# Optimization experiments

Measured on AMD Instinct MI355X. Metric: run time of the kernel, lower is better.

Reference implementation:

```python
import jax, jax.numpy as jnp
import numpy as np

# Model hyperparameters (from init_kwargs)
B, N, D = 64, 196, 768      # batch, patches, patch_dim
TKN = 768                   # token dim
QK = 64                     # per-head qk dim
H = 12                      # heads
HN = int(4.0 * TKN)         # Hopfield hidden = 3072
BETA = 1.0 / np.sqrt(QK)    # attn_beta default: 1/sqrt(qk_dim)
BLOCKS = 2
K_STEPS = 4                 # time_steps per block
EPS = 1e-5
ALPHA_RAW0 = float(np.log(np.exp(1.0) - 1.0))  # softplus^-1(alpha_init=1.0)


def setup_inputs() -> dict:
    key = jax.random.key(0)
    ks = jax.random.split(key, 8)
    sd = 0.02
    return {
        "x": jax.random.normal(ks[0], (B, N, D), dtype=jnp.float32),
        "W_enc": jax.random.normal(ks[1], (D, TKN), dtype=jnp.float32) * sd,
        "b_enc": jnp.zeros((TKN,), jnp.float32),
        "cls": jnp.ones((1, 1, TKN), jnp.float32),
        "pos": jax.random.normal(ks[2], (1, N + 1, TKN), dtype=jnp.float32) * sd,
        "gamma": jnp.ones((BLOCKS,), jnp.float32),             # EnergyLayerNorm scalar gain per block
        "bias": jnp.zeros((BLOCKS, TKN), jnp.float32),          # EnergyLayerNorm bias per block
        "Wq": jax.random.normal(ks[3], (BLOCKS, H, QK, TKN), dtype=jnp.float32) * sd,
        "Wk": jax.random.normal(ks[4], (BLOCKS, H, QK, TKN), dtype=jnp.float32) * sd,
        "Whn": jax.random.normal(ks[5], (BLOCKS, TKN, HN), dtype=jnp.float32) * sd,
        "alpha_raw": jnp.full((BLOCKS,), ALPHA_RAW0, jnp.float32),
        "ln_g": jnp.ones((TKN,), jnp.float32),
        "ln_b": jnp.zeros((TKN,), jnp.float32),
        "W_dec": jax.random.normal(ks[6], (TKN, D), dtype=jnp.float32) * sd,
        "b_dec": jnp.zeros((D,), jnp.float32),
    }


def _enorm(x, g_scale, g_bias):
    # EnergyLayerNorm: scalar gamma, per-dim bias, RMS of centered x
    xm = x - x.mean(-1, keepdims=True)
    return g_scale * xm * jax.lax.rsqrt((xm * xm).mean(-1, keepdims=True) + EPS) + g_bias


def _energy(g, Wq, Wk, Whn):
    # Hopfield-attention energy: -1/beta * sum logsumexp(beta * K^T Q)
    q = jnp.einsum("bnd,hzd->bnhz", g, Wq)
    k = jnp.einsum("bnd,hzd->bnhz", g, Wk)
    logits = jnp.einsum("bqhz,bkhz->bhqk", q, k)  # [B,H,N+1,N+1]
    e_attn = -(1.0 / BETA) * jnp.sum(jax.nn.logsumexp(BETA * logits, axis=-1))
    # Hopfield memory energy: -0.5 * sum relu(g W)^2
    e_hn = -0.5 * jnp.sum(jax.nn.relu(g @ Whn) ** 2)
    return e_attn + e_hn


_egrad = jax.grad(_energy)


def reference(x, W_enc, b_enc, cls, pos, gamma, bias, Wq, Wk, Whn, alpha_raw,
              ln_g, ln_b, W_dec, b_dec):
    t = x @ W_enc + b_enc                                   # encode -> [B,N,TKN]
    t = jnp.concatenate([jnp.broadcast_to(cls, (t.shape[0], 1, TKN)), t], axis=1)
    t = t + pos                                             # [B,N+1,TKN]
    for b in range(BLOCKS):
        a = jax.nn.softplus(alpha_raw[b])
        for _ in range(K_STEPS):
            g = _enorm(t, gamma[b], bias[b])
            t = t - a * _egrad(g, Wq[b], Wk[b], Whn[b])
    # decode: standard LayerNorm then Linear
    mu = t.mean(-1, keepdims=True)
    var = ((t - mu) ** 2).mean(-1, keepdims=True)
    h = (t - mu) * jax.lax.rsqrt(var + EPS) * ln_g + ln_b
    out = h @ W_dec + b_dec
    return out[:, 1:]                                       # drop CLS -> [B,N,D]
```

## Files before the change

### kernel.cpp

```cpp
#include <hip/hip_runtime.h>
#include <cstdint>
#include <cstddef>

using u16 = unsigned short;
typedef short short8 __attribute__((ext_vector_type(8)));
typedef short short4v __attribute__((ext_vector_type(4)));
typedef float f32x4 __attribute__((ext_vector_type(4)));

#define LN_EPS 1e-5f
#define ATT_BETA 0.125f

__device__ __forceinline__ u16 f2bf(float f){
  uint32_t u = __float_as_uint(f);
  u += 0x7fffu + ((u >> 16) & 1u);
  return (u16)(u >> 16);
}
__device__ __forceinline__ float bf2f(u16 h){
  return __uint_as_float(((uint32_t)h) << 16);
}
__device__ __forceinline__ float wred_sum(float v){
  #pragma unroll
  for(int o=32;o;o>>=1) v += __shfl_xor(v,o,64);
  return v;
}
__device__ __forceinline__ void async16(const void* g, void* l){
  __builtin_amdgcn_global_load_lds((const __attribute__((address_space(1))) void*)g,
                                   (__attribute__((address_space(3))) void*)l, 16, 0, 0);
}

template<int EPI, int ASPL>
__global__ __launch_bounds__(256)
void gemm_bt(const u16* __restrict__ A, const u16* __restrict__ A2,
             const u16* __restrict__ B,
             u16* __restrict__ Cb, float* __restrict__ Cf,
             int M, int N, int K, int ldb, int ldc,
             const float* __restrict__ aux0, const float* __restrict__ aux1,
             const float* __restrict__ araw, int blk)
{
  __shared__ u16 lA[128*32];
  __shared__ u16 lB[128*32];
  int tid = threadIdx.x;
  int w = tid >> 6, l = tid & 63;
  int wm = w >> 1, wn = w & 1;
  int m0 = blockIdx.y * 128, n0 = blockIdx.x * 128;
  int lr = l >> 2;
  int lc = (l & 3) * 8;
  f32x4 acc[4][4];
  #pragma unroll
  for(int i=0;i<4;i++)
    #pragma unroll
    for(int j=0;j<4;j++) acc[i][j] = (f32x4){0.f,0.f,0.f,0.f};
  int fm = l & 15, fq = (l >> 4) * 8;

  for(int kt=0; kt<K; kt+=32){
    __syncthreads();
    const u16* Asrc = A; int kcol = kt;
    if(ASPL){ if(kt >= 768){ Asrc = A2; kcol = kt - 768; } }
    int lda = ASPL ? 768 : K;
    #pragma unroll
    for(int c=0;c<2;c++){
      int rr = (w*2+c)*16;
      int ga = m0 + rr + lr; if(ga > M-1) ga = M-1;
      async16(Asrc + (size_t)ga*lda + kcol + lc, &lA[rr*32]);
      int gb = n0 + rr + lr; if(gb > N-1) gb = N-1;
      async16(B + (size_t)gb*ldb + kt + lc, &lB[rr*32]);
    }
    __syncthreads();
    short8 af[4], bfv[4];
    #pragma unroll
    for(int i=0;i<4;i++) af[i]  = *(const short8*)&lA[(wm*64 + i*16 + fm)*32 + fq];
    #pragma unroll
    for(int j=0;j<4;j++) bfv[j] = *(const short8*)&lB[(wn*64 + j*16 + fm)*32 + fq];
    #pragma unroll
    for(int i=0;i<4;i++)
      #pragma unroll
      for(int j=0;j<4;j++)
        acc[i][j] = __builtin_amdgcn_mfma_f32_16x16x32_bf16(af[i], bfv[j], acc[i][j], 0, 0, 0);
  }

  float alpha = 0.f;
  if(EPI==2) alpha = log1pf(__expf(araw[blk]));

  #pragma unroll
  for(int i=0;i<4;i++){
    int row_b = m0 + wm*64 + i*16 + (l>>4)*4;
    #pragma unroll
    for(int j=0;j<4;j++){
      int col = n0 + wn*64 + j*16 + (l&15);
      #pragma unroll
      for(int r=0;r<4;r++){
        int row = row_b + r;
        if(row >= M) continue;
        float v = acc[i][j][r];
        if(EPI==1){
          Cb[(size_t)row*ldc + col] = f2bf(v > 0.f ? v : 0.f);
        } else if(EPI==2){
          Cf[(size_t)row*768 + col] += alpha * v;
        } else if(EPI==3){
          int pb = row / 196, pn = row - pb*196;
          Cf[((size_t)pb*197 + 1 + pn)*768 + col] = v + aux0[col] + aux1[(size_t)(1+pn)*768 + col];
        } else {
          int pb = row / 197, rr2 = row - pb*197;
          if(rr2 > 0) Cf[((size_t)pb*196 + rr2 - 1)*768 + col] = v + aux0[col];
        }
      }
    }
  }
}

__global__ __launch_bounds__(256)
void norm_k(const float* __restrict__ t, u16* __restrict__ out,
            const float* __restrict__ gv, const float* __restrict__ bv, int blk, int mode)
{
  __shared__ float r1[4], r2[4];
  int row = blockIdx.x;
  const float* tr = t + (size_t)row*768;
  int tid = threadIdx.x, w = tid>>6, l = tid&63;
  f32x4 v = (f32x4){0.f,0.f,0.f,0.f};
  float s=0.f, s2=0.f;
  if(tid < 192){
    v = ((const f32x4*)tr)[tid];
    s  = v[0]+v[1]+v[2]+v[3];
    s2 = v[0]*v[0]+v[1]*v[1]+v[2]*v[2]+v[3]*v[3];
  }
  s = wred_sum(s); s2 = wred_sum(s2);
  if(l==0){ r1[w]=s; r2[w]=s2; }
  __syncthreads();
  s  = r1[0]+r1[1]+r1[2]+r1[3];
  s2 = r2[0]+r2[1]+r2[2]+r2[3];
  float mu  = s * (1.0f/768.0f);
  float var = s2 * (1.0f/768.0f) - mu*mu;
  float rs  = rsqrtf(var + LN_EPS);
  u16* orow = out + (size_t)row*768;
  if(tid < 192){
    short4v o;
    if(mode==0){
      float gm = gv[blk];
      const float* bb = bv + blk*768;
      #pragma unroll
      for(int c=0;c<4;c++) o[c] = (short)f2bf((v[c]-mu)*rs*gm + bb[tid*4+c]);
    } else {
      #pragma unroll
      for(int c=0;c<4;c++) o[c] = (short)f2bf((v[c]-mu)*rs*gv[tid*4+c] + bv[tid*4+c]);
    }
    ((short4v*)orow)[tid] = o;
  }
}

__global__ __launch_bounds__(512, 2)
void attn_fused(const u16* __restrict__ g, const u16* __restrict__ Wqk,
                u16* __restrict__ GqO, u16* __restrict__ GkO)
{
  __shared__ u16 smem[76800];
  __shared__ float SredS[2][4][16];
  u16* Qlds = smem;
  u16* Klds = smem + 14976;
  u16* QTl  = smem + 29952;
  u16* KTl  = smem + 44800;
  u16* P    = smem + 59648;
  u16* PT   = smem + 67840;
  u16* lg   = smem + 59648;

  int bhw = blockIdx.x;
  int bh = (bhw & 7)*96 + (bhw >> 3);
  int b = bh/12, h = bh - b*12;
  const u16* grows = g + (size_t)b*197*768;
  u16* Qg = GqO + (size_t)b*197*768 + h*64;
  u16* Kg = GkO + (size_t)b*197*768 + h*64;
  int tid = threadIdx.x, w = tid>>6, l = tid&63;
  int lane16 = l & 15, quad = l >> 4;

  for(int idx=tid; idx<64*24; idx+=512){
    int z = idx/24, c = 208 + (idx - (idx/24)*24);
    QTl[z*232 + c] = 0; KTl[z*232 + c] = 0;
  }

  {
    int half = w >> 2;
    int wsub = w & 3;
    int rt0 = (wsub==0) ? 0 : 1 + 3*wsub;
    int rtn = (wsub==0) ? 4 : 3;
    const u16* Wb = Wqk + (size_t)half*589824 + (size_t)(h*64)*768;
    u16* Lr = half ? Klds : Qlds;
    u16* Lt = half ? KTl  : QTl;
    f32x4 acc[4][4];
    #pragma unroll
    for(int i=0;i<4;i++)
      #pragma unroll
      for(int z=0;z<4;z++) acc[i][z] = (f32x4){0.f,0.f,0.f,0.f};

    #define STAGE_G(bufi, ktv) do{                                                   \
      int idx0 = tid;                                                                \
      { int rw = idx0>>2, c4 = idx0&3; int r2 = rw>196?196:rw;                       \
        async16(grows + (size_t)r2*768 + (ktv)*32 + c4*8, lg + (bufi)*6656 + idx0*8);}\
      int idx1 = tid + 512;                                                          \
      if(idx1 < 832){ int rw = idx1>>2, c4 = idx1&3; int r2 = rw>196?196:rw;         \
        async16(grows + (size_t)r2*768 + (ktv)*32 + c4*8, lg + (bufi)*6656 + idx1*8);}\
    }while(0)

    short8 bq[4], bqn[4];
    #pragma unroll
    for(int z=0;z<4;z++) bq[z] = *(const short8*)(Wb + (size_t)(z*16+lane16)*768 + quad*8);
    STAGE_G(0, 0);
    int buf = 0;
    for(int kt=0; kt<24; kt++){
      __syncthreads();
      if(kt < 23){
        STAGE_G(buf^1, kt+1);
        #pragma unroll
        for(int z=0;z<4;z++)
          bqn[z] = *(const short8*)(Wb + (size_t)(z*16+lane16)*768 + (kt+1)*32 + quad*8);
      }
      const u16* lb = lg + buf*6656;
      #pragma unroll
      for(int i=0;i<4;i++) if(i<rtn){
        short8 af = *(const short8*)(lb + (size_t)((rt0+i)*16 + lane16)*32 + quad*8);
        #pragma unroll
        for(int z=0;z<4;z++)
          acc[i][z] = __builtin_amdgcn_mfma_f32_16x16x32_bf16(af, bq[z], acc[i][z],0,0,0);
      }
      #pragma unroll
      for(int z=0;z<4;z++) bq[z] = bqn[z];
      buf ^= 1;
    }
    #undef STAGE_G

    #pragma unroll
    for(int i=0;i<4;i++) if(i<rtn)
      #pragma unroll
      for(int z=0;z<4;z++)
        #pragma unroll
        for(int r=0;r<4;r++){
          int q  = (rt0+i)*16 + quad*4 + r;
          int zz = z*16 + lane16;
          u16 hv = f2bf(acc[i][z][r]);
          Lr[q*72   + zz] = hv;
          Lt[zz*232 + q ] = hv;
        }
  }
  __syncthreads();

  int mt = w & 1, nh = w >> 1;
  int ncnt = (nh==0) ? 4 : 3;
  int nt0s = (nh==0) ? 0 : (1 + 3*nh);
  int jt0 = (w<5) ? 2*w : 10+(w-5);
  int jn  = (w<5) ? 2 : 1;

  f32x4 gk[2][4];
  #pragma unroll
  for(int a=0;a<2;a++)
    #pragma unroll
    for(int n2=0;n2<4;n2++) gk[a][n2] = (f32x4){0.f,0.f,0.f,0.f};

  for(int st=0; st<7; st++){
    int q0 = st*32;
    __syncthreads();
    int qa = q0 + 16*mt + lane16; if(qa > 196) qa = 196;
    short8 a0 = *(const short8*)&Qlds[qa*72 + quad*8];
    short8 a1 = *(const short8*)&Qlds[qa*72 + 32 + quad*8];
    f32x4 sa[4];
    #pragma unroll
    for(int ni=0;ni<4;ni++) sa[ni] = (f32x4){0.f,0.f,0.f,0.f};
    for(int ni=0; ni<ncnt; ni++){
      int jb = (nt0s+ni)*16 + lane16; if(jb > 196) jb = 196;
      short8 b0 = *(const short8*)&Klds[jb*72 + quad*8];
      short8 b1 = *(const short8*)&Klds[jb*72 + 32 + quad*8];
      sa[ni] = __builtin_amdgcn_mfma_f32_16x16x32_bf16(a0, b0, sa[ni],0,0,0);
      sa[ni] = __builtin_amdgcn_mfma_f32_16x16x32_bf16(a1, b1, sa[ni],0,0,0);
    }
    for(int ni=0; ni<ncnt; ni++){
      if((nt0s+ni)*16 + lane16 > 196){
        sa[ni][0]=-3e38f; sa[ni][1]=-3e38f; sa[ni][2]=-3e38f; sa[ni][3]=-3e38f;
      }
    }
    float ss[4] = {0.f,0.f,0.f,0.f};
    for(int ni=0; ni<ncnt; ni++)
      #pragma unroll
      for(int r=0;r<4;r++){
        float e = __expf(fminf(ATT_BETA*sa[ni][r], 80.f));
        sa[ni][r] = e; ss[r] += e;
      }
    #pragma unroll
    for(int o=1;o<16;o<<=1)
      #pragma unroll
      for(int r=0;r<4;r++) ss[r] += __shfl_xor(ss[r], o, 64);
    if(lane16==0){
      #pragma unroll
      for(int r=0;r<4;r++) SredS[mt][nh][quad*4+r] = ss[r];
    }
    __syncthreads();
    float inv[4];
    #pragma unroll
    for(int r=0;r<4;r++)
      inv[r] = 1.f/(SredS[mt][0][quad*4+r] + SredS[mt][1][quad*4+r]
                  + SredS[mt][2][quad*4+r] + SredS[mt][3][quad*4+r]);
    for(int ni=0; ni<ncnt; ni++){
      int j = (nt0s+ni)*16 + lane16;
      short4v pk;
      #pragma unroll
      for(int r=0;r<4;r++){
        int q = 16*mt + quad*4 + r;
        float val = (q0 + q <= 196) ? sa[ni][r]*inv[r] : 0.f;
        u16 hv = f2bf(val);
        P[q*256 + 8*((j>>3)^(q&7)) + (j&7)] = hv;
        pk[r] = (short)hv;
      }
      *(short4v*)&PT[j*40 + 16*mt + 4*quad] = pk;
    }
    for(int idx=tid; idx<32*16; idx+=512){
      int q = idx>>4, j = 208 + (idx&15);
      P[q*256 + 8*((j>>3)^(q&7)) + (j&7)] = 0;
    }
    __syncthreads();
    {
      f32x4 gq = (f32x4){0.f,0.f,0.f,0.f};
      int qrow = 16*mt + lane16;
      int z = nh*16 + lane16;
      for(int kt=0; kt<7; kt++){
        short8 af = *(const short8*)&P[qrow*256 + 8*((4*kt+quad)^(qrow&7))];
        short8 bf8 = *(const short8*)&KTl[z*232 + kt*32 + quad*8];
        gq = __builtin_amdgcn_mfma_f32_16x16x32_bf16(af, bf8, gq,0,0,0);
      }
      #pragma unroll
      for(int r=0;r<4;r++){
        int qg2 = q0 + 16*mt + quad*4 + r;
        if(qg2 <= 196) Qg[(size_t)qg2*768 + nh*16 + lane16] = f2bf(gq[r]);
      }
    }
    {
      short8 bq2[4];
      #pragma unroll
      for(int n2=0;n2<4;n2++)
        bq2[n2] = *(const short8*)&QTl[(n2*16+lane16)*232 + q0 + quad*8];
      for(int ji=0; ji<jn; ji++){
        int j = (jt0+ji)*16 + lane16;
        short8 af = *(const short8*)&PT[j*40 + quad*8];
        #pragma unroll
        for(int n2=0;n2<4;n2++)
          gk[ji][n2] = __builtin_amdgcn_mfma_f32_16x16x32_bf16(af, bq2[n2], gk[ji][n2],0,0,0);
      }
    }
  }
  __syncthreads();
  for(int ji=0; ji<jn; ji++){
    int jt = jt0 + ji;
    #pragma unroll
    for(int n2=0;n2<4;n2++)
      #pragma unroll
      for(int r=0;r<4;r++){
        int j = jt*16 + quad*4 + r;
        if(j <= 196) Kg[(size_t)j*768 + n2*16 + lane16] = f2bf(gk[ji][n2][r]);
      }
  }
}

__global__ void cvt_k(const float* __restrict__ in, u16* __restrict__ out, int n){
  for(int i=blockIdx.x*256+threadIdx.x; i<n; i+=gridDim.x*256) out[i] = f2bf(in[i]);
}

__global__ __launch_bounds__(256)
void tr_k(const float* __restrict__ src, u16* __restrict__ dst, int R, int C, int dstride, int coff){
  __shared__ float tile[32][33];
  int c0 = blockIdx.x*32, r0 = blockIdx.y*32;
  int tx = threadIdx.x & 31, ty = threadIdx.x >> 5;
  for(int i=ty;i<32;i+=8) tile[i][tx] = src[(size_t)(r0+i)*C + c0 + tx];
  __syncthreads();
  for(int i=ty;i<32;i+=8) dst[(size_t)(c0+i)*dstride + coff + r0 + tx] = f2bf(tile[tx][i]);
}

__global__ void fill_cls_k(float* __restrict__ t, const float* __restrict__ cls, const float* __restrict__ pos){
  int b = blockIdx.x;
  for(int i=threadIdx.x;i<768;i+=256) t[(size_t)b*197*768 + i] = cls[i] + pos[i];
}

extern "C" void kernel_launch(void* const* d_in, const int* in_sizes, int n_in,
                              void* d_out, int out_size, void* d_ws, size_t ws_size,
                              hipStream_t stream){
  const float* x      = (const float*)d_in[0];
  const float* W_enc  = (const float*)d_in[1];
  const float* b_enc  = (const float*)d_in[2];
  const float* cls    = (const float*)d_in[3];
  const float* pos    = (const float*)d_in[4];
  const float* gamma  = (const float*)d_in[5];
  const float* bias   = (const float*)d_in[6];
  const float* Wq     = (const float*)d_in[7];
  const float* Wk     = (const float*)d_in[8];
  const float* Whn    = (const float*)d_in[9];
  const float* araw   = (const float*)d_in[10];
  const float* ln_g   = (const float*)d_in[11];
  const float* ln_b   = (const float*)d_in[12];
  const float* W_dec  = (const float*)d_in[13];
  const float* b_dec  = (const float*)d_in[14];
  float* out = (float*)d_out;
  (void)in_sizes; (void)n_in; (void)out_size;

  const int M  = 64*197;
  const int MX = 64*196;

  char* p = (char*)d_ws;
  float* t   = (float*)p;  p += (size_t)M*768*4;
  u16*   g   = (u16*)p;    p += (size_t)M*768*2;
  u16*   Qb  = (u16*)p;    p += (size_t)M*768*2;
  u16*   Kb  = (u16*)p;    p += (size_t)M*768*2;
  size_t base = (size_t)(p - (char*)d_ws);
  if(base > ws_size) return;
  u16* hidden; int hop_merged;
  if(base + (size_t)M*3072*2 <= ws_size){ hidden = (u16*)(d_ws) + base/2; hop_merged = 1; }
  else { hidden = Qb; hop_merged = 0; }

  u16* Wall = (u16*)d_out;
  u16* Wqkb = Wall;
  u16* WqkT = Wall + 2359296;
  u16* WhnT = Wall + 4718592;
  u16* WhnB = Wall + 9437184;
  u16* xb    = Qb;
  u16* WencT = Kb;
  u16* WdecT = Kb;

  for(int b=0;b<2;b++){
    cvt_k<<<512,256,0,stream>>>(Wq + (size_t)b*589824, Wqkb + (size_t)b*1179648, 589824);
    cvt_k<<<512,256,0,stream>>>(Wk + (size_t)b*589824, Wqkb + (size_t)b*1179648 + 589824, 589824);
    tr_k<<<dim3(24,24),256,0,stream>>>(Wq + (size_t)b*589824, WqkT + (size_t)b*1179648, 768,768, 1536, 0);
    tr_k<<<dim3(24,24),256,0,stream>>>(Wk + (size_t)b*589824, WqkT + (size_t)b*1179648, 768,768, 1536, 768);
    tr_k<<<dim3(96,24),256,0,stream>>>(Whn + (size_t)b*2359296, WhnT + (size_t)b*2359296, 768,3072, 768, 0);
    cvt_k<<<2048,256,0,stream>>>(Whn + (size_t)b*2359296, WhnB + (size_t)b*2359296, 2359296);
  }

  cvt_k<<<1024,256,0,stream>>>(x, xb, MX*768);
  tr_k<<<dim3(24,24),256,0,stream>>>(W_enc, WencT, 768,768, 768, 0);
  fill_cls_k<<<64,256,0,stream>>>(t, cls, pos);
  gemm_bt<3,0><<<dim3(6,98),256,0,stream>>>(xb, nullptr, WencT, nullptr, t,
                                            MX, 768, 768, 768, 768,
                                            b_enc, pos, nullptr, 0);

  for(int blk=0; blk<2; blk++){
    for(int s=0; s<4; s++){
      norm_k<<<M,256,0,stream>>>(t, g, gamma, bias, blk, 0);
      if(hop_merged){
        gemm_bt<1,0><<<dim3(24,99),256,0,stream>>>(g, nullptr,
            WhnT + (size_t)blk*2359296,
            hidden, nullptr, M, 3072, 768, 768, 3072,
            nullptr, nullptr, nullptr, 0);
        gemm_bt<2,0><<<dim3(6,99),256,0,stream>>>(hidden, nullptr,
            WhnB + (size_t)blk*2359296,
            nullptr, t, M, 768, 3072, 3072, 768,
            nullptr, nullptr, araw, blk);
      } else {
        for(int c=0;c<2;c++){
          gemm_bt<1,0><<<dim3(12,99),256,0,stream>>>(g, nullptr,
              WhnT + (size_t)blk*2359296 + (size_t)c*1536*768,
              hidden, nullptr, M, 1536, 768, 768, 1536,
              nullptr, nullptr, nullptr, 0);
          gemm_bt<2,0><<<dim3(6,99),256,0,stream>>>(hidden, nullptr,
              WhnB + (size_t)blk*2359296 + (size_t)c*1536,
              nullptr, t, M, 768, 1536, 3072, 768,
              nullptr, nullptr, araw, blk);
        }
      }
      attn_fused<<<768,512,0,stream>>>(g, Wqkb + (size_t)blk*1179648, Qb, Kb);
      gemm_bt<2,1><<<dim3(6,99),256,0,stream>>>(Qb, Kb, WqkT + (size_t)blk*1179648,
            nullptr, t, M, 768, 1536, 1536, 768,
            nullptr, nullptr, araw, blk);
    }
  }

  tr_k<<<dim3(24,24),256,0,stream>>>(W_dec, WdecT, 768,768, 768, 0);
  norm_k<<<M,256,0,stream>>>(t, g, ln_g, ln_b, 0, 1);
  gemm_bt<4,0><<<dim3(6,99),256,0,stream>>>(g, nullptr, WdecT, nullptr, out,
                                            M, 768, 768, 768, 768,
                                            b_dec, nullptr, nullptr, 0);
}
```

Measured before the change: 4.211 ms.

## Widen fused attention kernel to 1024 threads and redistribute wave work

Doubles the attn_fused block from 8 to 16 waves and spreads the QK projection row tiles, score tiles and gradient work across more waves, so each wave holds fewer accumulators. The dQ and dK products now run on disjoint wave sets (waves 0-7 and 8-15) instead of every wave doing both. The P padding zeroing is hoisted out of the step loop. LDS use of about 150 KB per block still allows only one block per CU, so latency hiding depends on the extra waves inside a block, and the larger block makes each barrier cost more.

```diff
diff --git a/kernel.cpp b/kernel.cpp
--- a/kernel.cpp
+++ b/kernel.cpp
@@ -147,12 +147,12 @@
   }
 }
 
-__global__ __launch_bounds__(512, 2)
+__global__ __launch_bounds__(1024, 4)
 void attn_fused(const u16* __restrict__ g, const u16* __restrict__ Wqk,
                 u16* __restrict__ GqO, u16* __restrict__ GkO)
 {
   __shared__ u16 smem[76800];
-  __shared__ float SredS[2][4][16];
+  __shared__ float SredS[2][8][16];
   u16* Qlds = smem;
   u16* Klds = smem + 14976;
   u16* QTl  = smem + 29952;
@@ -170,32 +170,28 @@
   int tid = threadIdx.x, w = tid>>6, l = tid&63;
   int lane16 = l & 15, quad = l >> 4;
 
-  for(int idx=tid; idx<64*24; idx+=512){
+  for(int idx=tid; idx<64*24; idx+=1024){
     int z = idx/24, c = 208 + (idx - (idx/24)*24);
     QTl[z*232 + c] = 0; KTl[z*232 + c] = 0;
   }
 
   {
-    int half = w >> 2;
-    int wsub = w & 3;
-    int rt0 = (wsub==0) ? 0 : 1 + 3*wsub;
-    int rtn = (wsub==0) ? 4 : 3;
+    int half = w >> 3;
+    int wsub = w & 7;
+    int rt0 = (wsub<5) ? 2*wsub : 10+(wsub-5);
+    int rtn = (wsub<5) ? 2 : 1;
     const u16* Wb = Wqk + (size_t)half*589824 + (size_t)(h*64)*768;
     u16* Lr = half ? Klds : Qlds;
     u16* Lt = half ? KTl  : QTl;
-    f32x4 acc[4][4];
-    #pragma unroll
-    for(int i=0;i<4;i++)
+    f32x4 acc[2][4];
+    #pragma unroll
+    for(int i=0;i<2;i++)
       #pragma unroll
       for(int z=0;z<4;z++) acc[i][z] = (f32x4){0.f,0.f,0.f,0.f};
 
-    #define STAGE_G(bufi, ktv) do{                                                   \
-      int idx0 = tid;                                                                \
-      { int rw = idx0>>2, c4 = idx0&3; int r2 = rw>196?196:rw;                       \
-        async16(grows + (size_t)r2*768 + (ktv)*32 + c4*8, lg + (bufi)*6656 + idx0*8);}\
-      int idx1 = tid + 512;                                                          \
-      if(idx1 < 832){ int rw = idx1>>2, c4 = idx1&3; int r2 = rw>196?196:rw;         \
-        async16(grows + (size_t)r2*768 + (ktv)*32 + c4*8, lg + (bufi)*6656 + idx1*8);}\
+    #define STAGE_G(bufi, ktv) do{                                                    \
+      if(tid < 832){ int rw = tid>>2, c4 = tid&3; int r2 = rw>196?196:rw;             \
+        async16(grows + (size_t)r2*768 + (ktv)*32 + c4*8, lg + (bufi)*6656 + tid*8);} \
     }while(0)
 
     short8 bq[4], bqn[4];
@@ -213,7 +209,7 @@
       }
       const u16* lb = lg + buf*6656;
       #pragma unroll
-      for(int i=0;i<4;i++) if(i<rtn){
+      for(int i=0;i<2;i++) if(i<rtn){
         short8 af = *(const short8*)(lb + (size_t)((rt0+i)*16 + lane16)*32 + quad*8);
         #pragma unroll
         for(int z=0;z<4;z++)
@@ -226,7 +222,7 @@
     #undef STAGE_G
 
     #pragma unroll
-    for(int i=0;i<4;i++) if(i<rtn)
+    for(int i=0;i<2;i++) if(i<rtn)
       #pragma unroll
       for(int z=0;z<4;z++)
         #pragma unroll
@@ -240,11 +236,17 @@
   }
   __syncthreads();
 
-  int mt = w & 1, nh = w >> 1;
-  int ncnt = (nh==0) ? 4 : 3;
-  int nt0s = (nh==0) ? 0 : (1 + 3*nh);
-  int jt0 = (w<5) ? 2*w : 10+(w-5);
-  int jn  = (w<5) ? 2 : 1;
+  if(tid < 512){
+    int q = tid>>4, j = 208 + (tid&15);
+    P[q*256 + 8*((j>>3)^(q&7)) + (j&7)] = 0;
+  }
+
+  int smt = w & 1, snh = w >> 1;
+  int ncnt = (snh<5) ? 2 : 1;
+  int nt0s = (snh<5) ? 2*snh : 10+(snh-5);
+  int w8 = w - 8;
+  int jt0 = 0, jn = 0;
+  if(w >= 8){ jt0 = (w8<5) ? 2*w8 : 10+(w8-5); jn = (w8<5) ? 2 : 1; }
 
   f32x4 gk[2][4];
   #pragma unroll
@@ -255,12 +257,12 @@
   for(int st=0; st<7; st++){
     int q0 = st*32;
     __syncthreads();
-    int qa = q0 + 16*mt + lane16; if(qa > 196) qa = 196;
+    int qa = q0 + 16*smt + lane16; if(qa > 196) qa = 196;
     short8 a0 = *(const short8*)&Qlds[qa*72 + quad*8];
     short8 a1 = *(const short8*)&Qlds[qa*72 + 32 + quad*8];
-    f32x4 sa[4];
-    #pragma unroll
-    for(int ni=0;ni<4;ni++) sa[ni] = (f32x4){0.f,0.f,0.f,0.f};
+    f32x4 sa[2];
+    #pragma unroll
+    for(int ni=0;ni<2;ni++) sa[ni] = (f32x4){0.f,0.f,0.f,0.f};
     for(int ni=0; ni<ncnt; ni++){
       int jb = (nt0s+ni)*16 + lane16; if(jb > 196) jb = 196;
       short8 b0 = *(const short8*)&Klds[jb*72 + quad*8];
@@ -286,33 +288,33 @@
       for(int r=0;r<4;r++) ss[r] += __shfl_xor(ss[r], o, 64);
     if(lane16==0){
       #pragma unroll
-      for(int r=0;r<4;r++) SredS[mt][nh][quad*4+r] = ss[r];
+      for(int r=0;r<4;r++) SredS[smt][snh][quad*4+r] = ss[r];
     }
     __syncthreads();
     float inv[4];
     #pragma unroll
-    for(int r=0;r<4;r++)
-      inv[r] = 1.f/(SredS[mt][0][quad*4+r] + SredS[mt][1][quad*4+r]
-                  + SredS[mt][2][quad*4+r] + SredS[mt][3][quad*4+r]);
+    for(int r=0;r<4;r++){
+      float sr = 0.f;
+      #pragma unroll
+      for(int pp=0; pp<8; pp++) sr += SredS[smt][pp][quad*4+r];
+      inv[r] = 1.f/sr;
+    }
     for(int ni=0; ni<ncnt; ni++){
       int j = (nt0s+ni)*16 + lane16;
       short4v pk;
       #pragma unroll
       for(int r=0;r<4;r++){
-        int q = 16*mt + quad*4 + r;
+        int q = 16*smt + quad*4 + r;
         float val = (q0 + q <= 196) ? sa[ni][r]*inv[r] : 0.f;
         u16 hv = f2bf(val);
         P[q*256 + 8*((j>>3)^(q&7)) + (j&7)] = hv;
         pk[r] = (short)hv;
       }
-      *(short4v*)&PT[j*40 + 16*mt + 4*quad] = pk;
-    }
-    for(int idx=tid; idx<32*16; idx+=512){
-      int q = idx>>4, j = 208 + (idx&15);
-      P[q*256 + 8*((j>>3)^(q&7)) + (j&7)] = 0;
+      *(short4v*)&PT[j*40 + 16*smt + 4*quad] = pk;
     }
     __syncthreads();
-    {
+    if(w < 8){
+      int mt = w & 1, nh = w >> 1;
       f32x4 gq = (f32x4){0.f,0.f,0.f,0.f};
       int qrow = 16*mt + lane16;
       int z = nh*16 + lane16;
@@ -327,7 +329,7 @@
         if(qg2 <= 196) Qg[(size_t)qg2*768 + nh*16 + lane16] = f2bf(gq[r]);
       }
     }
-    {
+    if(jn){
       short8 bq2[4];
       #pragma unroll
       for(int n2=0;n2<4;n2++)
@@ -457,7 +459,7 @@
               nullptr, nullptr, araw, blk);
         }
       }
-      attn_fused<<<768,512,0,stream>>>(g, Wqkb + (size_t)blk*1179648, Qb, Kb);
+      attn_fused<<<768,1024,0,stream>>>(g, Wqkb + (size_t)blk*1179648, Qb, Kb);
       gemm_bt<2,1><<<dim3(6,99),256,0,stream>>>(Qb, Kb, WqkT + (size_t)blk*1179648,
             nullptr, t, M, 768, 1536, 1536, 768,
             nullptr, nullptr, araw, blk);
```

Result: slower. 4.992 ms (+18.5%).
